# Kernel tuning notes

Measured on AMD Instinct MI355X. Metric: run time of the kernel, lower is better.

## Reference

```python
import jax, jax.numpy as jnp
import numpy as np

N = 20000
E = 320000
IN = 256
H = 4
C = 64
NEG_SLOPE = 0.2


def setup_inputs() -> dict:
    key = jax.random.key(0)
    ks = jax.random.split(key, 12)
    HC = H * C

    def w(k, shape, fan_in):
        return jax.random.normal(k, shape, dtype=jnp.float32) / np.sqrt(fan_in)

    x = jax.random.normal(ks[0], (N, IN), dtype=jnp.float32)
    edge_index = jax.random.randint(ks[1], (2, E), 0, N, dtype=jnp.int64)
    return {
        "x": x,
        "edge_index": edge_index,
        "Wl1": w(ks[2], (IN, HC), IN),
        "Wr1": w(ks[3], (IN, HC), IN),
        "att1": w(ks[4], (H, C), C),
        "b1": jnp.zeros((HC,), dtype=jnp.float32),
        "Wl2": w(ks[5], (HC, HC), HC),
        "Wr2": w(ks[6], (HC, HC), HC),
        "att2": w(ks[7], (H, C), C),
        "b2": jnp.zeros((HC,), dtype=jnp.float32),
        "Wfc": w(ks[8], (HC, 2), HC),
        "bfc": jnp.zeros((2,), dtype=jnp.float32),
    }


def _gatv2(x, src, dst, Wl, Wr, att, b):
    """GATv2Conv (concat=True, share_weights=False), inference (no dropout)."""
    n = x.shape[0]
    xl = (x @ Wl).reshape(n, H, C)  # source-side projection
    xr = (x @ Wr).reshape(n, H, C)  # target-side projection
    # per-edge GATv2 score: a^T LeakyReLU(xl_j + xr_i)
    e = jax.nn.leaky_relu(xl[src] + xr[dst], NEG_SLOPE)      # [E, H, C]
    score = jnp.einsum("ehc,hc->eh", e, att)                 # [E, H]
    # segment softmax over incoming edges of each target node
    smax = jax.ops.segment_max(score, dst, num_segments=n)   # [N, H]
    ex = jnp.exp(score - smax[dst])
    denom = jax.ops.segment_sum(ex, dst, num_segments=n)     # [N, H]
    alpha = ex / denom[dst]                                  # [E, H]
    # scatter-aggregate messages (source projections weighted by alpha)
    out = jax.ops.segment_sum(alpha[:, :, None] * xl[src], dst, num_segments=n)
    return out.reshape(n, H * C) + b


def reference(x, edge_index, Wl1, Wr1, att1, b1, Wl2, Wr2, att2, b2, Wfc, bfc):
    n = x.shape[0]
    # add_self_loops=True (PyG default)
    loop = jnp.arange(n, dtype=edge_index.dtype)
    src = jnp.concatenate([edge_index[0], loop])
    dst = jnp.concatenate([edge_index[1], loop])

    h = _gatv2(x, src, dst, Wl1, Wr1, att1, b1)
    h = jax.nn.relu(h)
    h = _gatv2(h, src, dst, Wl2, Wr2, att2, b2)
    h = jax.nn.relu(h)
    g = jnp.mean(h, axis=0, keepdims=True)  # [1, H*C]
    return g @ Wfc + bfc                    # [1, 2]
```

## Files before the change

### kernel.cpp

```cpp
#include <hip/hip_runtime.h>
#include <hip/hip_bf16.h>
#include <math.h>

#define Nn 20000
#define Ee 320000
#define INF_ 256
#define Hh 4
#define Cc 64
#define HC 256
#define NEG_SLOPE 0.2f

using frag16 = __attribute__((ext_vector_type(8))) short;
using f32x4  = __attribute__((ext_vector_type(4))) float;

__device__ __forceinline__ void async16(const void* g, void* l) {
    __builtin_amdgcn_global_load_lds(
        (const __attribute__((address_space(1))) unsigned int*)g,
        (__attribute__((address_space(3))) unsigned int*)l,
        16, 0, 0);
}


__global__ void init_deg(int* deg, int n) {
    int i = blockIdx.x * blockDim.x + threadIdx.x;
    if (i < n) deg[i] = 1;
}

__global__ void hist_kernel(const int* __restrict__ dst, int ne, int* deg) {
    int e = blockIdx.x * blockDim.x + threadIdx.x;
    if (e < ne) atomicAdd(&deg[dst[e]], 1);
}

__global__ __launch_bounds__(256) void scan1(const int* __restrict__ deg,
                                             int* __restrict__ excl,
                                             int* __restrict__ bsum, int n) {
    int tid = threadIdx.x;
    int gid = blockIdx.x * 256 + tid;
    int lane = tid & 63;
    int v = (gid < n) ? deg[gid] : 0;
    int x = v;
    #pragma unroll
    for (int off = 1; off < 64; off <<= 1) {
        int y = __shfl_up(x, off, 64);
        if (lane >= off) x += y;
    }
    __shared__ int wsum[4];
    if (lane == 63) wsum[tid >> 6] = x;
    __syncthreads();
    int wadd = 0;
    for (int w = 0; w < (tid >> 6); ++w) wadd += wsum[w];
    int incl = x + wadd;
    if (gid < n) excl[gid] = incl - v;
    if (tid == 255) bsum[blockIdx.x] = incl;
}

__global__ void scan2(const int* __restrict__ bsum, int* __restrict__ boff, int nb) {
    int lane = threadIdx.x;
    int carry = 0;
    for (int base = 0; base < nb; base += 64) {
        int i = base + lane;
        int v = (i < nb) ? bsum[i] : 0;
        int x = v;
        #pragma unroll
        for (int off = 1; off < 64; off <<= 1) {
            int y = __shfl_up(x, off, 64);
            if (lane >= off) x += y;
        }
        if (i < nb) boff[i] = carry + x - v;
        carry += __shfl(x, 63, 64);
    }
    if (lane == 0) boff[nb] = carry;
}

__global__ void scan_add(int* __restrict__ row_start, int* __restrict__ cursor,
                         const int* __restrict__ boff, int n, int nb) {
    int gid = blockIdx.x * blockDim.x + threadIdx.x;
    if (gid < n) {
        int v = row_start[gid] + boff[gid >> 8];
        row_start[gid] = v;
        cursor[gid] = v;
    }
    if (gid == n) row_start[n] = boff[nb];
}

__global__ void scatter_kernel(const int* __restrict__ src, const int* __restrict__ dst,
                               int ne, int n, int* cursor, int* colx) {
    int e = blockIdx.x * blockDim.x + threadIdx.x;
    if (e < ne) {
        int d = dst[e];
        int pos = atomicAdd(&cursor[d], 1);
        colx[pos] = src[e];
    } else if (e < ne + n) {
        int node = e - ne;
        int pos = atomicAdd(&cursor[node], 1);
        colx[pos] = node;
    }
}


__device__ inline unsigned short bf16rn(float f) {
    unsigned u = __float_as_uint(f);
    unsigned r = (u + 0x7FFFu + ((u >> 16) & 1u)) >> 16;
    return (unsigned short)r;
}

__device__ inline void split1(float v, short& h, short& l) {
    unsigned short hh = bf16rn(v);
    float back = __uint_as_float(((unsigned)hh) << 16);
    unsigned short ll = bf16rn(v - back);
    h = (short)hh; l = (short)ll;
}

__device__ __forceinline__ float4 bf4_to_f4(ushort4 u) {
    return make_float4(__uint_as_float((unsigned)u.x << 16),
                       __uint_as_float((unsigned)u.y << 16),
                       __uint_as_float((unsigned)u.z << 16),
                       __uint_as_float((unsigned)u.w << 16));
}

__global__ __launch_bounds__(256) void split_kernel(const float* __restrict__ in,
                                                    short* __restrict__ hi,
                                                    short* __restrict__ lo, int n4) {
    int i = blockIdx.x * blockDim.x + threadIdx.x;
    if (i >= n4) return;
    float4 v = ((const float4*)in)[i];
    short4 h, l;
    split1(v.x, h.x, l.x);
    split1(v.y, h.y, l.y);
    split1(v.z, h.z, l.z);
    split1(v.w, h.w, l.w);
    ((short4*)hi)[i] = h;
    ((short4*)lo)[i] = l;
}

__global__ __launch_bounds__(256) void wsplit_all(const float* __restrict__ Wl1,
                                                  const float* __restrict__ Wr1,
                                                  const float* __restrict__ Wl2,
                                                  const float* __restrict__ Wr2,
                                                  short* __restrict__ WhT1,
                                                  short* __restrict__ WlT1,
                                                  short* __restrict__ WhT2,
                                                  short* __restrict__ WlT2) {
    int b = blockIdx.x;
    int n = b & 255;
    int k = threadIdx.x;
    const float* W = (b < 256) ? Wl1 : (b < 512) ? Wr1 : (b < 768) ? Wl2 : Wr2;
    short* Wh = (b < 512) ? WhT1 : WhT2;
    short* Wl = (b < 512) ? WlT1 : WlT2;
    int col = b & 511;
    float v = W[k * 256 + n];
    short h, l;
    split1(v, h, l);
    Wh[col * 256 + k] = h;
    Wl[col * 256 + k] = l;
}


#define BK 32

__global__ __launch_bounds__(256) void mfma_gemm(const short* __restrict__ Ah,
                                                 const short* __restrict__ Al,
                                                 const short* __restrict__ WhT,
                                                 const short* __restrict__ WlT,
                                                 unsigned short* __restrict__ XLh,
                                                 float* __restrict__ XR) {
    __shared__ short As_h[128 * BK];
    __shared__ short As_l[128 * BK];
    __shared__ short Bs_h[128 * BK];
    __shared__ short Bs_l[128 * BK];
    int tid = threadIdx.x;
    int wave = tid >> 6, lane = tid & 63;
    int quad = lane >> 4, lc = lane & 15;
    int bx = blockIdx.x;
    int bm = blockIdx.y * 128;
    int cbase = (bx * 128) & 255;

    int sr0 = wave * 32 + (lane >> 2);
    int sr1 = sr0 + 16;
    int koff = (lane & 3) * 8;
    int ga0 = bm + sr0; if (ga0 >= Nn) ga0 = Nn - 1;
    int ga1 = bm + sr1; if (ga1 >= Nn) ga1 = Nn - 1;
    int gb0 = bx * 128 + sr0;
    int gb1 = bx * 128 + sr1;
    int j0 = wave * 2, j1 = j0 + 1;

    f32x4 acc[2][8] = {};
    for (int c = 0; c < 8; ++c) {
        int k0 = c * BK;
        async16(Ah  + (size_t)ga0 * HC + k0 + koff, &As_h[j0 * 512]);
        async16(Ah  + (size_t)ga1 * HC + k0 + koff, &As_h[j1 * 512]);
        async16(Al  + (size_t)ga0 * HC + k0 + koff, &As_l[j0 * 512]);
        async16(Al  + (size_t)ga1 * HC + k0 + koff, &As_l[j1 * 512]);
        async16(WhT + (size_t)gb0 * HC + k0 + koff, &Bs_h[j0 * 512]);
        async16(WhT + (size_t)gb1 * HC + k0 + koff, &Bs_h[j1 * 512]);
        async16(WlT + (size_t)gb0 * HC + k0 + koff, &Bs_l[j0 * 512]);
        async16(WlT + (size_t)gb1 * HC + k0 + koff, &Bs_l[j1 * 512]);
        __syncthreads();

        frag16 a0h = *(const frag16*)&As_h[(wave * 32 + lc) * BK + quad * 8];
        frag16 a1h = *(const frag16*)&As_h[(wave * 32 + 16 + lc) * BK + quad * 8];
        frag16 a0l = *(const frag16*)&As_l[(wave * 32 + lc) * BK + quad * 8];
        frag16 a1l = *(const frag16*)&As_l[(wave * 32 + 16 + lc) * BK + quad * 8];
        #pragma unroll
        for (int t = 0; t < 8; ++t) {
            frag16 bh = *(const frag16*)&Bs_h[(t * 16 + lc) * BK + quad * 8];
            frag16 bl = *(const frag16*)&Bs_l[(t * 16 + lc) * BK + quad * 8];
            acc[0][t] = __builtin_amdgcn_mfma_f32_16x16x32_bf16(a0h, bh, acc[0][t], 0, 0, 0);
            acc[1][t] = __builtin_amdgcn_mfma_f32_16x16x32_bf16(a1h, bh, acc[1][t], 0, 0, 0);
            acc[0][t] = __builtin_amdgcn_mfma_f32_16x16x32_bf16(a0l, bh, acc[0][t], 0, 0, 0);
            acc[1][t] = __builtin_amdgcn_mfma_f32_16x16x32_bf16(a1l, bh, acc[1][t], 0, 0, 0);
            acc[0][t] = __builtin_amdgcn_mfma_f32_16x16x32_bf16(a0h, bl, acc[0][t], 0, 0, 0);
            acc[1][t] = __builtin_amdgcn_mfma_f32_16x16x32_bf16(a1h, bl, acc[1][t], 0, 0, 0);
        }
        __syncthreads();
    }
    #pragma unroll
    for (int mt = 0; mt < 2; ++mt) {
        int rbase = bm + wave * 32 + mt * 16 + quad * 4;
        #pragma unroll
        for (int t = 0; t < 8; ++t) {
            int col = cbase + t * 16 + lc;
            #pragma unroll
            for (int r = 0; r < 4; ++r) {
                int rw = rbase + r;
                if (rw >= Nn) continue;
                if (bx < 2) XLh[(size_t)rw * HC + col] = bf16rn(acc[mt][t][r]);
                else        XR [(size_t)rw * HC + col] = acc[mt][t][r];
            }
        }
    }
}


__device__ __forceinline__ float edge_score(const float4 v, const float4 xr,
                                            const float4 a06, const float4 a04) {
    float tx = v.x + xr.x, ty = v.y + xr.y, tz = v.z + xr.z, tw = v.w + xr.w;
    float p = a06.x * tx + a04.x * fabsf(tx);
    p += a06.y * ty + a04.y * fabsf(ty);
    p += a06.z * tz + a04.z * fabsf(tz);
    p += a06.w * tw + a04.w * fabsf(tw);
    p += __shfl_xor(p, 1, 64);
    p += __shfl_xor(p, 2, 64);
    p += __shfl_xor(p, 4, 64);
    p += __shfl_xor(p, 8, 64);
    return p;
}

__global__ __launch_bounds__(256) void gat_kernel(const ushort4* __restrict__ XL4,
                                                  const float4* __restrict__ XR4,
                                                  const int* __restrict__ row_start,
                                                  const int* __restrict__ colx,
                                                  const float4* __restrict__ att4,
                                                  const float4* __restrict__ bias4,
                                                  float4* __restrict__ Hout,
                                                  short4* __restrict__ Ahi,
                                                  short4* __restrict__ Alo,
                                                  int mode) {
    int wave = threadIdx.x >> 6, lane = threadIdx.x & 63;
    int node = blockIdx.x * 4 + wave;
    float4 xr = XR4[(size_t)node * 64 + lane];
    float4 a  = att4[lane];
    float4 a06 = make_float4(a.x * 0.6f, a.y * 0.6f, a.z * 0.6f, a.w * 0.6f);
    float4 a04 = make_float4(a.x * 0.4f, a.y * 0.4f, a.z * 0.4f, a.w * 0.4f);
    int e0 = row_start[node], e1 = row_start[node + 1];
    float l0 = 0.f, l1 = 0.f;
    float4 acc0 = make_float4(0.f, 0.f, 0.f, 0.f);
    float4 acc1 = make_float4(0.f, 0.f, 0.f, 0.f);
    int e = e0;
    for (; e + 1 < e1; e += 2) {
        int s0 = __builtin_amdgcn_readfirstlane(colx[e]);
        int s1 = __builtin_amdgcn_readfirstlane(colx[e + 1]);
        ushort4 u0 = XL4[(size_t)s0 * 64 + lane];
        ushort4 u1 = XL4[(size_t)s1 * 64 + lane];
        float4 v0 = bf4_to_f4(u0);
        float4 v1 = bf4_to_f4(u1);
        float pe0 = __expf(edge_score(v0, xr, a06, a04));
        float pe1 = __expf(edge_score(v1, xr, a06, a04));
        l0 += pe0; l1 += pe1;
        acc0.x += pe0 * v0.x; acc0.y += pe0 * v0.y;
        acc0.z += pe0 * v0.z; acc0.w += pe0 * v0.w;
        acc1.x += pe1 * v1.x; acc1.y += pe1 * v1.y;
        acc1.z += pe1 * v1.z; acc1.w += pe1 * v1.w;
    }
    if (e < e1) {
        int s0 = __builtin_amdgcn_readfirstlane(colx[e]);
        float4 v0 = bf4_to_f4(XL4[(size_t)s0 * 64 + lane]);
        float pe0 = __expf(edge_score(v0, xr, a06, a04));
        l0 += pe0;
        acc0.x += pe0 * v0.x; acc0.y += pe0 * v0.y;
        acc0.z += pe0 * v0.z; acc0.w += pe0 * v0.w;
    }
    float rl = 1.f / (l0 + l1);
    float4 b = bias4[lane];
    float4 o = make_float4(fmaxf((acc0.x + acc1.x) * rl + b.x, 0.f),
                           fmaxf((acc0.y + acc1.y) * rl + b.y, 0.f),
                           fmaxf((acc0.z + acc1.z) * rl + b.z, 0.f),
                           fmaxf((acc0.w + acc1.w) * rl + b.w, 0.f));
    size_t oidx = (size_t)node * 64 + lane;
    if (mode) {
        short4 h4, l4;
        split1(o.x, h4.x, l4.x);
        split1(o.y, h4.y, l4.y);
        split1(o.z, h4.z, l4.z);
        split1(o.w, h4.w, l4.w);
        Ahi[oidx] = h4;
        Alo[oidx] = l4;
    } else {
        Hout[oidx] = o;
    }
}


__global__ void zero_f(float* p, int n) {
    int i = blockIdx.x * blockDim.x + threadIdx.x;
    if (i < n) p[i] = 0.f;
}

__global__ __launch_bounds__(256) void colsum_kernel(const float* __restrict__ Hmat,
                                                     float* __restrict__ g, int n) {
    int ch = threadIdx.x;
    float s = 0.f;
    for (int r = blockIdx.x; r < n; r += gridDim.x)
        s += Hmat[(size_t)r * HC + ch];
    atomicAdd(&g[ch], s);
}

__global__ __launch_bounds__(256) void fc_kernel(const float* __restrict__ g,
                                                 const float* __restrict__ Wfc,
                                                 const float* __restrict__ bfc,
                                                 float* __restrict__ out, float invN) {
    int t = threadIdx.x;
    float gv = g[t] * invN;
    float p0 = gv * Wfc[2 * t];
    float p1 = gv * Wfc[2 * t + 1];
    #pragma unroll
    for (int off = 32; off > 0; off >>= 1) {
        p0 += __shfl_xor(p0, off, 64);
        p1 += __shfl_xor(p1, off, 64);
    }
    __shared__ float s0[4], s1[4];
    if ((t & 63) == 0) { s0[t >> 6] = p0; s1[t >> 6] = p1; }
    __syncthreads();
    if (t == 0) {
        out[0] = s0[0] + s0[1] + s0[2] + s0[3] + bfc[0];
        out[1] = s1[0] + s1[1] + s1[2] + s1[3] + bfc[1];
    }
}


extern "C" void kernel_launch(void* const* d_in, const int* in_sizes, int n_in,
                              void* d_out, int out_size, void* d_ws, size_t ws_size,
                              hipStream_t stream) {
    const float* x    = (const float*)d_in[0];
    const int*   eidx = (const int*)d_in[1];
    const float* Wl1  = (const float*)d_in[2];
    const float* Wr1  = (const float*)d_in[3];
    const float* att1 = (const float*)d_in[4];
    const float* b1   = (const float*)d_in[5];
    const float* Wl2  = (const float*)d_in[6];
    const float* Wr2  = (const float*)d_in[7];
    const float* att2 = (const float*)d_in[8];
    const float* b2   = (const float*)d_in[9];
    const float* Wfc  = (const float*)d_in[10];
    const float* bfc  = (const float*)d_in[11];
    float* out = (float*)d_out;

    const int* srcv = eidx;
    const int* dstv = eidx + Ee;

    size_t NHC = (size_t)Nn * HC;
    float* XR = (float*)d_ws;
    float* Hb = XR + NHC;
    float* g  = Hb + NHC;
    unsigned short* XLh = (unsigned short*)(g + HC);
    short* Ah   = (short*)(XLh + NHC);
    short* Al   = Ah + NHC;
    short* WhT1 = Al + NHC;
    short* WlT1 = WhT1 + 512 * 256;
    short* WhT2 = WlT1 + 512 * 256;
    short* WlT2 = WhT2 + 512 * 256;
    int* deg       = (int*)(WlT2 + 512 * 256);
    int* row_start = deg + Nn;
    int* cursor    = row_start + (Nn + 1);
    int* colx      = cursor + Nn;
    int* bsum      = colx + (Ee + Nn);
    int* boff      = bsum + 128;

    const int NB = (Nn + 255) / 256;
    const int N4 = (int)(NHC / 4);

    init_deg<<<(Nn + 255) / 256, 256, 0, stream>>>(deg, Nn);
    hist_kernel<<<(Ee + 255) / 256, 256, 0, stream>>>(dstv, Ee, deg);
    scan1<<<NB, 256, 0, stream>>>(deg, row_start, bsum, Nn);
    scan2<<<1, 64, 0, stream>>>(bsum, boff, NB);
    scan_add<<<(Nn + 256) / 256, 256, 0, stream>>>(row_start, cursor, boff, Nn, NB);
    scatter_kernel<<<(Ee + Nn + 255) / 256, 256, 0, stream>>>(srcv, dstv, Ee, Nn, cursor, colx);

    dim3 ggrid(4, (Nn + 127) / 128);

    wsplit_all<<<1024, 256, 0, stream>>>(Wl1, Wr1, Wl2, Wr2, WhT1, WlT1, WhT2, WlT2);
    split_kernel<<<(N4 + 255) / 256, 256, 0, stream>>>(x, Ah, Al, N4);

    mfma_gemm<<<ggrid, 256, 0, stream>>>(Ah, Al, WhT1, WlT1, XLh, XR);
    gat_kernel<<<Nn / 4, 256, 0, stream>>>((const ushort4*)XLh, (const float4*)XR,
                                           row_start, colx, (const float4*)att1,
                                           (const float4*)b1, (float4*)Hb,
                                           (short4*)Ah, (short4*)Al, 1);

    mfma_gemm<<<ggrid, 256, 0, stream>>>(Ah, Al, WhT2, WlT2, XLh, XR);
    gat_kernel<<<Nn / 4, 256, 0, stream>>>((const ushort4*)XLh, (const float4*)XR,
                                           row_start, colx, (const float4*)att2,
                                           (const float4*)b2, (float4*)Hb,
                                           (short4*)Ah, (short4*)Al, 0);

    zero_f<<<1, 256, 0, stream>>>(g, HC);
    colsum_kernel<<<256, 256, 0, stream>>>(Hb, g, Nn);
    fc_kernel<<<1, 256, 0, stream>>>(g, Wfc, bfc, out, 1.0f / Nn);
}
```

Measured before the change: 296.1 us.

## Fuse CSR build into cooperative kernel, merge prep and tail kernels, unroll GAT loop

Replaces the six CSR-construction launches with one cooperative kernel that uses grid-wide syncs between the histogram, scan and scatter phases, and also zeroes the pooling accumulator and a completion counter. The weight split and input split kernels become one launch, and colsum plus fc become one kernel where the last block to finish does the final projection. The GAT edge loop goes from 2 to 4 independent edges per iteration to keep more gathers in flight. These changes cut launch count and latency at the cost of grid.sync overhead, a small 256-block grid for the atomics-heavy phases, and more registers in the GAT kernel.

```diff
diff --git a/kernel.cpp b/kernel.cpp
--- a/kernel.cpp
+++ b/kernel.cpp
@@ -1,6 +1,9 @@
 #include <hip/hip_runtime.h>
+#include <hip/hip_cooperative_groups.h>
 #include <hip/hip_bf16.h>
 #include <math.h>
+
+namespace cg = cooperative_groups;
 
 #define Nn 20000
 #define Ee 320000
@@ -9,6 +12,7 @@
 #define Cc 64
 #define HC 256
 #define NEG_SLOPE 0.2f
+#define NB 79
 
 using frag16 = __attribute__((ext_vector_type(8))) short;
 using f32x4  = __attribute__((ext_vector_type(4))) float;
@@ -21,138 +25,143 @@
 }
 
 
-__global__ void init_deg(int* deg, int n) {
-    int i = blockIdx.x * blockDim.x + threadIdx.x;
-    if (i < n) deg[i] = 1;
-}
-
-__global__ void hist_kernel(const int* __restrict__ dst, int ne, int* deg) {
-    int e = blockIdx.x * blockDim.x + threadIdx.x;
-    if (e < ne) atomicAdd(&deg[dst[e]], 1);
-}
-
-__global__ __launch_bounds__(256) void scan1(const int* __restrict__ deg,
-                                             int* __restrict__ excl,
-                                             int* __restrict__ bsum, int n) {
+__device__ inline unsigned short bf16rn(float f) {
+    unsigned u = __float_as_uint(f);
+    unsigned r = (u + 0x7FFFu + ((u >> 16) & 1u)) >> 16;
+    return (unsigned short)r;
+}
+
+__device__ inline void split1(float v, short& h, short& l) {
+    unsigned short hh = bf16rn(v);
+    float back = __uint_as_float(((unsigned)hh) << 16);
+    unsigned short ll = bf16rn(v - back);
+    h = (short)hh; l = (short)ll;
+}
+
+__device__ __forceinline__ float4 bf4_to_f4(ushort4 u) {
+    return make_float4(__uint_as_float((unsigned)u.x << 16),
+                       __uint_as_float((unsigned)u.y << 16),
+                       __uint_as_float((unsigned)u.z << 16),
+                       __uint_as_float((unsigned)u.w << 16));
+}
+
+
+__global__ __launch_bounds__(256) void csr_coop(const int* __restrict__ srcv,
+                                                const int* __restrict__ dstv,
+                                                int* deg, int* row_start,
+                                                int* cursor, int* colx,
+                                                int* bsum, int* boff,
+                                                float* g, int* fcnt) {
+    cg::grid_group grid = cg::this_grid();
     int tid = threadIdx.x;
     int gid = blockIdx.x * 256 + tid;
-    int lane = tid & 63;
-    int v = (gid < n) ? deg[gid] : 0;
-    int x = v;
-    #pragma unroll
-    for (int off = 1; off < 64; off <<= 1) {
-        int y = __shfl_up(x, off, 64);
-        if (lane >= off) x += y;
-    }
+    const int GSZ = 256 * 256;
+
+    if (gid < Nn) deg[gid] = 1;
+    if (gid < HC) g[gid] = 0.f;
+    if (gid == 0) *fcnt = 0;
+    grid.sync();
+
+    for (int e = gid; e < Ee; e += GSZ) atomicAdd(&deg[dstv[e]], 1);
+    grid.sync();
+
     __shared__ int wsum[4];
-    if (lane == 63) wsum[tid >> 6] = x;
-    __syncthreads();
-    int wadd = 0;
-    for (int w = 0; w < (tid >> 6); ++w) wadd += wsum[w];
-    int incl = x + wadd;
-    if (gid < n) excl[gid] = incl - v;
-    if (tid == 255) bsum[blockIdx.x] = incl;
-}
-
-__global__ void scan2(const int* __restrict__ bsum, int* __restrict__ boff, int nb) {
-    int lane = threadIdx.x;
-    int carry = 0;
-    for (int base = 0; base < nb; base += 64) {
-        int i = base + lane;
-        int v = (i < nb) ? bsum[i] : 0;
+    if (blockIdx.x < NB) {
+        int lane = tid & 63;
+        int v = (gid < Nn) ? deg[gid] : 0;
         int x = v;
         #pragma unroll
         for (int off = 1; off < 64; off <<= 1) {
             int y = __shfl_up(x, off, 64);
             if (lane >= off) x += y;
         }
-        if (i < nb) boff[i] = carry + x - v;
-        carry += __shfl(x, 63, 64);
-    }
-    if (lane == 0) boff[nb] = carry;
-}
-
-__global__ void scan_add(int* __restrict__ row_start, int* __restrict__ cursor,
-                         const int* __restrict__ boff, int n, int nb) {
-    int gid = blockIdx.x * blockDim.x + threadIdx.x;
-    if (gid < n) {
+        if (lane == 63) wsum[tid >> 6] = x;
+        __syncthreads();
+        int wadd = 0;
+        for (int w = 0; w < (tid >> 6); ++w) wadd += wsum[w];
+        int incl = x + wadd;
+        if (gid < Nn) row_start[gid] = incl - v;
+        if (tid == 255) bsum[blockIdx.x] = incl;
+    }
+    grid.sync();
+
+    if (blockIdx.x == 0 && tid < 64) {
+        int lane = tid;
+        int carry = 0;
+        for (int base = 0; base < NB; base += 64) {
+            int i = base + lane;
+            int v = (i < NB) ? bsum[i] : 0;
+            int x = v;
+            #pragma unroll
+            for (int off = 1; off < 64; off <<= 1) {
+                int y = __shfl_up(x, off, 64);
+                if (lane >= off) x += y;
+            }
+            if (i < NB) boff[i] = carry + x - v;
+            carry += __shfl(x, 63, 64);
+        }
+        if (lane == 0) boff[NB] = carry;
+    }
+    grid.sync();
+
+    if (gid < Nn) {
         int v = row_start[gid] + boff[gid >> 8];
         row_start[gid] = v;
         cursor[gid] = v;
     }
-    if (gid == n) row_start[n] = boff[nb];
-}
-
-__global__ void scatter_kernel(const int* __restrict__ src, const int* __restrict__ dst,
-                               int ne, int n, int* cursor, int* colx) {
-    int e = blockIdx.x * blockDim.x + threadIdx.x;
-    if (e < ne) {
-        int d = dst[e];
-        int pos = atomicAdd(&cursor[d], 1);
-        colx[pos] = src[e];
-    } else if (e < ne + n) {
-        int node = e - ne;
-        int pos = atomicAdd(&cursor[node], 1);
-        colx[pos] = node;
-    }
-}
-
-
-__device__ inline unsigned short bf16rn(float f) {
-    unsigned u = __float_as_uint(f);
-    unsigned r = (u + 0x7FFFu + ((u >> 16) & 1u)) >> 16;
-    return (unsigned short)r;
-}
-
-__device__ inline void split1(float v, short& h, short& l) {
-    unsigned short hh = bf16rn(v);
-    float back = __uint_as_float(((unsigned)hh) << 16);
-    unsigned short ll = bf16rn(v - back);
-    h = (short)hh; l = (short)ll;
-}
-
-__device__ __forceinline__ float4 bf4_to_f4(ushort4 u) {
-    return make_float4(__uint_as_float((unsigned)u.x << 16),
-                       __uint_as_float((unsigned)u.y << 16),
-                       __uint_as_float((unsigned)u.z << 16),
-                       __uint_as_float((unsigned)u.w << 16));
-}
-
-__global__ __launch_bounds__(256) void split_kernel(const float* __restrict__ in,
-                                                    short* __restrict__ hi,
-                                                    short* __restrict__ lo, int n4) {
-    int i = blockIdx.x * blockDim.x + threadIdx.x;
-    if (i >= n4) return;
-    float4 v = ((const float4*)in)[i];
-    short4 h, l;
-    split1(v.x, h.x, l.x);
-    split1(v.y, h.y, l.y);
-    split1(v.z, h.z, l.z);
-    split1(v.w, h.w, l.w);
-    ((short4*)hi)[i] = h;
-    ((short4*)lo)[i] = l;
-}
-
-__global__ __launch_bounds__(256) void wsplit_all(const float* __restrict__ Wl1,
-                                                  const float* __restrict__ Wr1,
-                                                  const float* __restrict__ Wl2,
-                                                  const float* __restrict__ Wr2,
-                                                  short* __restrict__ WhT1,
-                                                  short* __restrict__ WlT1,
-                                                  short* __restrict__ WhT2,
-                                                  short* __restrict__ WlT2) {
+    if (gid == Nn) row_start[Nn] = boff[NB];
+    grid.sync();
+
+    for (int e = gid; e < Ee + Nn; e += GSZ) {
+        if (e < Ee) {
+            int d = dstv[e];
+            int pos = atomicAdd(&cursor[d], 1);
+            colx[pos] = srcv[e];
+        } else {
+            int node = e - Ee;
+            int pos = atomicAdd(&cursor[node], 1);
+            colx[pos] = node;
+        }
+    }
+}
+
+
+__global__ __launch_bounds__(256) void prep_kernel(const float* __restrict__ x,
+                                                   const float* __restrict__ Wl1,
+                                                   const float* __restrict__ Wr1,
+                                                   const float* __restrict__ Wl2,
+                                                   const float* __restrict__ Wr2,
+                                                   short* __restrict__ WhT1,
+                                                   short* __restrict__ WlT1,
+                                                   short* __restrict__ WhT2,
+                                                   short* __restrict__ WlT2,
+                                                   short* __restrict__ Ah,
+                                                   short* __restrict__ Al, int n4) {
     int b = blockIdx.x;
-    int n = b & 255;
-    int k = threadIdx.x;
-    const float* W = (b < 256) ? Wl1 : (b < 512) ? Wr1 : (b < 768) ? Wl2 : Wr2;
-    short* Wh = (b < 512) ? WhT1 : WhT2;
-    short* Wl = (b < 512) ? WlT1 : WlT2;
-    int col = b & 511;
-    float v = W[k * 256 + n];
-    short h, l;
-    split1(v, h, l);
-    Wh[col * 256 + k] = h;
-    Wl[col * 256 + k] = l;
+    if (b < 1024) {
+        int n = b & 255;
+        int k = threadIdx.x;
+        const float* W = (b < 256) ? Wl1 : (b < 512) ? Wr1 : (b < 768) ? Wl2 : Wr2;
+        short* Wh = (b < 512) ? WhT1 : WhT2;
+        short* Wl = (b < 512) ? WlT1 : WlT2;
+        int col = b & 511;
+        float v = W[k * 256 + n];
+        short h, l;
+        split1(v, h, l);
+        Wh[col * 256 + k] = h;
+        Wl[col * 256 + k] = l;
+    } else {
+        int i = (b - 1024) * 256 + threadIdx.x;
+        if (i >= n4) return;
+        float4 v = ((const float4*)x)[i];
+        short4 h, l;
+        split1(v.x, h.x, l.x);
+        split1(v.y, h.y, l.y);
+        split1(v.z, h.z, l.z);
+        split1(v.w, h.w, l.w);
+        ((short4*)Ah)[i] = h;
+        ((short4*)Al)[i] = l;
+    }
 }
 
 
@@ -263,26 +272,32 @@
     float4 a06 = make_float4(a.x * 0.6f, a.y * 0.6f, a.z * 0.6f, a.w * 0.6f);
     float4 a04 = make_float4(a.x * 0.4f, a.y * 0.4f, a.z * 0.4f, a.w * 0.4f);
     int e0 = row_start[node], e1 = row_start[node + 1];
-    float l0 = 0.f, l1 = 0.f;
+    float l0 = 0.f, l1 = 0.f, l2 = 0.f, l3 = 0.f;
     float4 acc0 = make_float4(0.f, 0.f, 0.f, 0.f);
     float4 acc1 = make_float4(0.f, 0.f, 0.f, 0.f);
+    float4 acc2 = make_float4(0.f, 0.f, 0.f, 0.f);
+    float4 acc3 = make_float4(0.f, 0.f, 0.f, 0.f);
     int e = e0;
-    for (; e + 1 < e1; e += 2) {
+    for (; e + 3 < e1; e += 4) {
         int s0 = __builtin_amdgcn_readfirstlane(colx[e]);
         int s1 = __builtin_amdgcn_readfirstlane(colx[e + 1]);
-        ushort4 u0 = XL4[(size_t)s0 * 64 + lane];
-        ushort4 u1 = XL4[(size_t)s1 * 64 + lane];
-        float4 v0 = bf4_to_f4(u0);
-        float4 v1 = bf4_to_f4(u1);
+        int s2 = __builtin_amdgcn_readfirstlane(colx[e + 2]);
+        int s3 = __builtin_amdgcn_readfirstlane(colx[e + 3]);
+        float4 v0 = bf4_to_f4(XL4[(size_t)s0 * 64 + lane]);
+        float4 v1 = bf4_to_f4(XL4[(size_t)s1 * 64 + lane]);
+        float4 v2 = bf4_to_f4(XL4[(size_t)s2 * 64 + lane]);
+        float4 v3 = bf4_to_f4(XL4[(size_t)s3 * 64 + lane]);
         float pe0 = __expf(edge_score(v0, xr, a06, a04));
         float pe1 = __expf(edge_score(v1, xr, a06, a04));
-        l0 += pe0; l1 += pe1;
-        acc0.x += pe0 * v0.x; acc0.y += pe0 * v0.y;
-        acc0.z += pe0 * v0.z; acc0.w += pe0 * v0.w;
-        acc1.x += pe1 * v1.x; acc1.y += pe1 * v1.y;
-        acc1.z += pe1 * v1.z; acc1.w += pe1 * v1.w;
-    }
-    if (e < e1) {
+        float pe2 = __expf(edge_score(v2, xr, a06, a04));
+        float pe3 = __expf(edge_score(v3, xr, a06, a04));
+        l0 += pe0; l1 += pe1; l2 += pe2; l3 += pe3;
+        acc0.x += pe0 * v0.x; acc0.y += pe0 * v0.y; acc0.z += pe0 * v0.z; acc0.w += pe0 * v0.w;
+        acc1.x += pe1 * v1.x; acc1.y += pe1 * v1.y; acc1.z += pe1 * v1.z; acc1.w += pe1 * v1.w;
+        acc2.x += pe2 * v2.x; acc2.y += pe2 * v2.y; acc2.z += pe2 * v2.z; acc2.w += pe2 * v2.w;
+        acc3.x += pe3 * v3.x; acc3.y += pe3 * v3.y; acc3.z += pe3 * v3.z; acc3.w += pe3 * v3.w;
+    }
+    for (; e < e1; ++e) {
         int s0 = __builtin_amdgcn_readfirstlane(colx[e]);
         float4 v0 = bf4_to_f4(XL4[(size_t)s0 * 64 + lane]);
         float pe0 = __expf(edge_score(v0, xr, a06, a04));
@@ -290,12 +305,12 @@
         acc0.x += pe0 * v0.x; acc0.y += pe0 * v0.y;
         acc0.z += pe0 * v0.z; acc0.w += pe0 * v0.w;
     }
-    float rl = 1.f / (l0 + l1);
+    float rl = 1.f / (l0 + l1 + l2 + l3);
     float4 b = bias4[lane];
-    float4 o = make_float4(fmaxf((acc0.x + acc1.x) * rl + b.x, 0.f),
-                           fmaxf((acc0.y + acc1.y) * rl + b.y, 0.f),
-                           fmaxf((acc0.z + acc1.z) * rl + b.z, 0.f),
-                           fmaxf((acc0.w + acc1.w) * rl + b.w, 0.f));
+    float4 o = make_float4(fmaxf((acc0.x + acc1.x + acc2.x + acc3.x) * rl + b.x, 0.f),
+                           fmaxf((acc0.y + acc1.y + acc2.y + acc3.y) * rl + b.y, 0.f),
+                           fmaxf((acc0.z + acc1.z + acc2.z + acc3.z) * rl + b.z, 0.f),
+                           fmaxf((acc0.w + acc1.w + acc2.w + acc3.w) * rl + b.w, 0.f));
     size_t oidx = (size_t)node * 64 + lane;
     if (mode) {
         short4 h4, l4;
@@ -311,37 +326,34 @@
 }
 
 
-__global__ void zero_f(float* p, int n) {
-    int i = blockIdx.x * blockDim.x + threadIdx.x;
-    if (i < n) p[i] = 0.f;
-}
-
-__global__ __launch_bounds__(256) void colsum_kernel(const float* __restrict__ Hmat,
-                                                     float* __restrict__ g, int n) {
-    int ch = threadIdx.x;
-    float s = 0.f;
-    for (int r = blockIdx.x; r < n; r += gridDim.x)
-        s += Hmat[(size_t)r * HC + ch];
-    atomicAdd(&g[ch], s);
-}
-
-__global__ __launch_bounds__(256) void fc_kernel(const float* __restrict__ g,
+__global__ __launch_bounds__(256) void colsum_fc(const float* __restrict__ Hmat,
+                                                 float* __restrict__ g,
+                                                 int* __restrict__ fcnt,
                                                  const float* __restrict__ Wfc,
                                                  const float* __restrict__ bfc,
                                                  float* __restrict__ out, float invN) {
-    int t = threadIdx.x;
-    float gv = g[t] * invN;
-    float p0 = gv * Wfc[2 * t];
-    float p1 = gv * Wfc[2 * t + 1];
+    int ch = threadIdx.x;
+    float s = 0.f;
+    for (int r = blockIdx.x; r < Nn; r += gridDim.x)
+        s += Hmat[(size_t)r * HC + ch];
+    atomicAdd(&g[ch], s);
+    __threadfence();
+    __shared__ int last;
+    if (ch == 0) last = (atomicAdd(fcnt, 1) == (int)gridDim.x - 1);
+    __syncthreads();
+    if (!last) return;
+    float gv = atomicAdd(&g[ch], 0.f) * invN;
+    float p0 = gv * Wfc[2 * ch];
+    float p1 = gv * Wfc[2 * ch + 1];
     #pragma unroll
     for (int off = 32; off > 0; off >>= 1) {
         p0 += __shfl_xor(p0, off, 64);
         p1 += __shfl_xor(p1, off, 64);
     }
     __shared__ float s0[4], s1[4];
-    if ((t & 63) == 0) { s0[t >> 6] = p0; s1[t >> 6] = p1; }
+    if ((ch & 63) == 0) { s0[ch >> 6] = p0; s1[ch >> 6] = p1; }
     __syncthreads();
-    if (t == 0) {
+    if (ch == 0) {
         out[0] = s0[0] + s0[1] + s0[2] + s0[3] + bfc[0];
         out[1] = s1[0] + s1[1] + s1[2] + s1[3] + bfc[1];
     }
@@ -385,21 +397,23 @@
     int* colx      = cursor + Nn;
     int* bsum      = colx + (Ee + Nn);
     int* boff      = bsum + 128;
-
-    const int NB = (Nn + 255) / 256;
+    int* fcnt      = boff + 128;
+
     const int N4 = (int)(NHC / 4);
 
-    init_deg<<<(Nn + 255) / 256, 256, 0, stream>>>(deg, Nn);
-    hist_kernel<<<(Ee + 255) / 256, 256, 0, stream>>>(dstv, Ee, deg);
-    scan1<<<NB, 256, 0, stream>>>(deg, row_start, bsum, Nn);
-    scan2<<<1, 64, 0, stream>>>(bsum, boff, NB);
-    scan_add<<<(Nn + 256) / 256, 256, 0, stream>>>(row_start, cursor, boff, Nn, NB);
-    scatter_kernel<<<(Ee + Nn + 255) / 256, 256, 0, stream>>>(srcv, dstv, Ee, Nn, cursor, colx);
+    {
+        void* args[] = { (void*)&srcv, (void*)&dstv, (void*)&deg, (void*)&row_start,
+                         (void*)&cursor, (void*)&colx, (void*)&bsum, (void*)&boff,
+                         (void*)&g, (void*)&fcnt };
+        hipLaunchCooperativeKernel((const void*)csr_coop, dim3(256), dim3(256),
+                                   args, 0, stream);
+    }
+
+    prep_kernel<<<1024 + N4 / 256, 256, 0, stream>>>(x, Wl1, Wr1, Wl2, Wr2,
+                                                     WhT1, WlT1, WhT2, WlT2,
+                                                     Ah, Al, N4);
 
     dim3 ggrid(4, (Nn + 127) / 128);
-
-    wsplit_all<<<1024, 256, 0, stream>>>(Wl1, Wr1, Wl2, Wr2, WhT1, WlT1, WhT2, WlT2);
-    split_kernel<<<(N4 + 255) / 256, 256, 0, stream>>>(x, Ah, Al, N4);
 
     mfma_gemm<<<ggrid, 256, 0, stream>>>(Ah, Al, WhT1, WlT1, XLh, XR);
     gat_kernel<<<Nn / 4, 256, 0, stream>>>((const ushort4*)XLh, (const float4*)XR,
@@ -413,7 +427,5 @@
                                            (const float4*)b2, (float4*)Hb,
                                            (short4*)Ah, (short4*)Al, 0);
 
-    zero_f<<<1, 256, 0, stream>>>(g, HC);
-    colsum_kernel<<<256, 256, 0, stream>>>(Hb, g, Nn);
-    fc_kernel<<<1, 256, 0, stream>>>(g, Wfc, bfc, out, 1.0f / Nn);
-}
+    colsum_fc<<<256, 256, 0, stream>>>(Hb, g, fcnt, Wfc, bfc, out, 1.0f / Nn);
+}
```

New measurement: 474.5 us. +60.3%, slower.
